# Optimization experiments

Measured on AMD Instinct MI355X. Metric: run time of the kernel, lower is better.

The kernel has to match this reference:

```python
import jax, jax.numpy as jnp
import numpy as np

OUTERCUTOFF = 5.0  # seqm_parameters['pair_outer_cutoff']
LENGTH_CONV = 1.8897261258369282  # Angstrom -> Bohr (constants.length_conversion_factor)
NMOL, MOLSIZE = 1024, 128


def setup_inputs() -> dict:
    key = jax.random.key(0)
    k1, k2 = jax.random.split(key)
    species = jax.random.randint(k1, (NMOL, MOLSIZE), 0, 9).astype(jnp.int32)
    coordinates = jax.random.uniform(k2, (NMOL, MOLSIZE, 3), dtype=jnp.float32) * 20.0
    # core charges indexed by atomic number (0=blank, H=1, ..., F=9)
    tore = jnp.array([0.0, 1.0, 0.0, 1.0, 2.0, 3.0, 4.0, 5.0, 6.0, 7.0], dtype=jnp.float32)
    return {"species": species, "coordinates": coordinates, "tore": tore}


def reference(species, coordinates, tore):
    nmol, molsize = species.shape
    nonblank = species > 0                               # (nmol, molsize)
    flat_nb = nonblank.reshape(-1)
    atom_index = jnp.arange(nmol * molsize, dtype=jnp.int32)
    real_atoms = atom_index[flat_nb]                     # compaction (eager, data-dependent)
    n_real = real_atoms.shape[0]
    inv_real_atoms = jnp.zeros((nmol * molsize,), jnp.int32).at[real_atoms].set(
        jnp.arange(n_real, dtype=jnp.int32))
    Z = species.reshape(-1)[real_atoms]
    nHeavy = jnp.sum(species > 1, axis=1)
    nHydro = jnp.sum(species == 1, axis=1)
    nocc = (jnp.sum(tore[species], axis=1) / 2.0).reshape(-1).astype(jnp.int32)
    t1 = (jnp.arange(molsize, dtype=jnp.int32) * (molsize + 1))[None, :]
    t2 = (jnp.arange(nmol, dtype=jnp.int32) * molsize ** 2)[:, None]
    maskd = (t1 + t2).reshape(-1)[real_atoms]
    atom_molid = jnp.repeat(jnp.arange(nmol, dtype=jnp.int32), molsize)[flat_nb]
    # pair bookkeeping: [i, a, b] with first=atom a, second=atom b
    nonblank_pairs = (nonblank[:, None, :] & nonblank[:, :, None]).reshape(-1)
    ai = atom_index.reshape(nmol, molsize)
    pair_first = jnp.broadcast_to(ai[:, :, None], (nmol, molsize, molsize)).reshape(-1)
    pair_second = jnp.broadcast_to(ai[:, None, :], (nmol, molsize, molsize)).reshape(-1)
    # paircoord_raw[i, a, b] = coord[i, b] - coord[i, a]
    paircoord_raw = (coordinates[:, None, :, :] - coordinates[:, :, None, :]).reshape(-1, 3)
    pairdist_raw = jnp.linalg.norm(paircoord_raw, axis=1)
    close_pairs = pairdist_raw < OUTERCUTOFF
    pairs = (pair_first < pair_second) & nonblank_pairs & close_pairs
    pidx = jnp.where(pairs)[0]
    paircoord = paircoord_raw[pidx]
    pairdist = pairdist_raw[pidx]
    rij = pairdist * LENGTH_CONV
    idxi = inv_real_atoms[pair_first[pidx]]
    idxj = inv_real_atoms[pair_second[pidx]]
    ni = Z[idxi]
    nj = Z[idxj]
    xij = paircoord / pairdist[:, None]
    mask = real_atoms[idxi] * molsize + real_atoms[idxj] % molsize
    pair_molid = atom_molid[idxi]
    return (nmol, molsize, nHeavy, nHydro, nocc, Z, maskd, atom_molid,
            mask, pair_molid, ni, nj, idxi, idxj, xij, rij)
```

## Files before the change

### kernel.cpp

```cpp
#include <hip/hip_runtime.h>
#include <hip/hip_bf16.h>

#define NMOL 1024
#define MOLSIZE 128


__device__ __forceinline__ float pair_dist(float ax, float ay, float az,
                                           float bx, float by, float bz,
                                           float& dx, float& dy, float& dz) {
    dx = __fsub_rn(bx, ax);
    dy = __fsub_rn(by, ay);
    dz = __fsub_rn(bz, az);
    float d2 = __fadd_rn(__fadd_rn(__fmul_rn(dx, dx), __fmul_rn(dy, dy)), __fmul_rn(dz, dz));
    return __fsqrt_rn(d2);
}

__global__ __launch_bounds__(256) void k_count(const int* __restrict__ species,
                                               const float* __restrict__ coord,
                                               const float* __restrict__ tore,
                                               float* __restrict__ out,
                                               int* __restrict__ cnt_real,
                                               int* __restrict__ pair_tot,
                                               unsigned long long* __restrict__ bal_g) {
    __shared__ float cx[MOLSIZE], cy[MOLSIZE], cz[MOLSIZE];
    __shared__ unsigned long long bal_s[256];
    __shared__ int sH[2], sY[2], sN[2];
    __shared__ float sT[2];
    __shared__ int wpair[4];
    int m = blockIdx.x, t = threadIdx.x;
    int lane = t & 63, w = t >> 6;
    if (t < MOLSIZE) {
        int f = m * MOLSIZE + t;
        int s = species[f];
        bool nb = (s > 0);
        float x = coord[3 * f + 0], y = coord[3 * f + 1], z = coord[3 * f + 2];
        float sent = 1.0e30f * (float)(t + 1);
        cx[t] = nb ? x : sent;
        cy[t] = nb ? y : sent;
        cz[t] = nb ? z : sent;
        int h = (s > 1) ? 1 : 0, yy = (s == 1) ? 1 : 0, nn = nb ? 1 : 0;
        float tv = tore[s];
        for (int d = 32; d > 0; d >>= 1) {
            h += __shfl_down(h, d);
            yy += __shfl_down(yy, d);
            nn += __shfl_down(nn, d);
            tv += __shfl_down(tv, d);
        }
        if (lane == 0) { sH[w] = h; sY[w] = yy; sN[w] = nn; sT[w] = tv; }
    }
    __syncthreads();
    if (t == 0) {
        out[2 + m] = (float)(sH[0] + sH[1]);
        out[2 + NMOL + m] = (float)(sY[0] + sY[1]);
        out[2 + 2 * NMOL + m] = (float)((int)((sT[0] + sT[1]) * 0.5f));
        cnt_real[m] = sN[0] + sN[1];
        if (m == 0) { out[0] = (float)NMOL; out[1] = (float)MOLSIZE; }
    }
    float bxl = cx[lane], byl = cy[lane], bzl = cz[lane];
    float bxh = cx[64 + lane], byh = cy[64 + lane], bzh = cz[64 + lane];
    int wcount = 0;
    for (int j = 0; j < 32; ++j) {
        int a = w + 4 * j;
        float ax = cx[a], ay = cy[a], az = cz[a];
        unsigned long long mb0 = 0ull, mb1 = 0ull;
        if (a < 63) {
            float dx, dy, dz;
            float dist = pair_dist(ax, ay, az, bxl, byl, bzl, dx, dy, dz);
            mb0 = __ballot((lane > a) && (dist < 5.0f));
        }
        if (a < 127) {
            float dx, dy, dz;
            float dist = pair_dist(ax, ay, az, bxh, byh, bzh, dx, dy, dz);
            mb1 = __ballot(((64 + lane) > a) && (dist < 5.0f));
        }
        if (lane == 0) { bal_s[2 * a] = mb0; bal_s[2 * a + 1] = mb1; }
        wcount += __popcll(mb0) + __popcll(mb1);
    }
    if (lane == 0) wpair[w] = wcount;
    __syncthreads();
    if (t == 0) pair_tot[m] = wpair[0] + wpair[1] + wpair[2] + wpair[3];
    bal_g[m * 256 + t] = bal_s[t];
}

__global__ __launch_bounds__(256) void k_scatter(const int* __restrict__ species,
                                                 const float* __restrict__ coord,
                                                 const int* __restrict__ cnt_real,
                                                 const int* __restrict__ pair_tot,
                                                 const unsigned long long* __restrict__ bal_g,
                                                 float* __restrict__ out) {
    __shared__ float cx[MOLSIZE], cy[MOLSIZE], cz[MOLSIZE], spf[MOLSIZE];
    __shared__ int iv[MOLSIZE];
    __shared__ unsigned long long bal_s[256];
    __shared__ int sIncl[256];
    __shared__ int wtot[4];
    __shared__ int redALT[4], redAALL[4], redPLT[4], redPALL[4];
    __shared__ int wc0s;
    int m = blockIdx.x, t = threadIdx.x;
    int lane = t & 63, w = t >> 6;

    unsigned long long bal = bal_g[m * 256 + t];
    bal_s[t] = bal;

    int4 ca = ((const int4*)cnt_real)[t];
    int4 cp = ((const int4*)pair_tot)[t];
    int i0 = 4 * t;
    int aLT = ((i0 + 0) < m ? ca.x : 0) + ((i0 + 1) < m ? ca.y : 0) +
              ((i0 + 2) < m ? ca.z : 0) + ((i0 + 3) < m ? ca.w : 0);
    int aALL = ca.x + ca.y + ca.z + ca.w;
    int pLT = ((i0 + 0) < m ? cp.x : 0) + ((i0 + 1) < m ? cp.y : 0) +
              ((i0 + 2) < m ? cp.z : 0) + ((i0 + 3) < m ? cp.w : 0);
    int pALL = cp.x + cp.y + cp.z + cp.w;
    for (int d = 32; d > 0; d >>= 1) {
        aLT += __shfl_down(aLT, d);
        aALL += __shfl_down(aALL, d);
        pLT += __shfl_down(pLT, d);
        pALL += __shfl_down(pALL, d);
    }
    if (lane == 0) { redALT[w] = aLT; redAALL[w] = aALL; redPLT[w] = pLT; redPALL[w] = pALL; }

    int s_at = 0;
    unsigned long long amb = 0ull;
    if (t < MOLSIZE) {
        int f = m * MOLSIZE + t;
        s_at = species[f];
        cx[t] = coord[3 * f + 0];
        cy[t] = coord[3 * f + 1];
        cz[t] = coord[3 * f + 2];
        spf[t] = (float)s_at;
        amb = __ballot(s_at > 0);
        if (t == 0) wc0s = __popcll(amb);
    }
    int v = __popcll(bal);
    int cval = v;
    for (int d = 1; d < 64; d <<= 1) {
        int u = __shfl_up(v, d);
        if (lane >= d) v += u;
    }
    (void)cval;
    if (lane == 63) wtot[w] = v;
    __syncthreads();

    int mol_base_m = redALT[0] + redALT[1] + redALT[2] + redALT[3];
    int n_real     = redAALL[0] + redAALL[1] + redAALL[2] + redAALL[3];
    int qbase      = redPLT[0] + redPLT[1] + redPLT[2] + redPLT[3];
    int npairs     = redPALL[0] + redPALL[1] + redPALL[2] + redPALL[3];

    if (t < MOLSIZE && s_at > 0) {
        int rank = __popcll(amb & ((1ull << lane) - 1ull)) + ((w == 1) ? wc0s : 0);
        int g = mol_base_m + rank;
        iv[t] = g;
        out[3074 + g] = (float)s_at;
        out[3074 + n_real + g] = (float)(t * (MOLSIZE + 1) + m * (MOLSIZE * MOLSIZE));
        out[3074 + 2 * n_real + g] = (float)m;
    }
    int add = 0;
    for (int ww = 0; ww < w; ++ww) add += wtot[ww];
    sIncl[t] = v + add;
    __syncthreads();
    int np_mol = sIncl[255];

    int offP = 3074 + 3 * n_real;
    float* pm0 = out + offP;
    float* pm1 = pm0 + npairs;
    float* pm2 = pm1 + npairs;
    float* pm3 = pm2 + npairs;
    float* pm4 = pm3 + npairs;
    float* pm5 = pm4 + npairs;
    float* px  = pm5 + npairs;
    float* pr  = px + 3 * npairs;
    float fm = (float)m;

    for (int q = t; q < np_mol; q += 256) {
        int c = 0;
        if (sIncl[c + 127] <= q) c += 128;
        if (sIncl[c + 63] <= q) c += 64;
        if (sIncl[c + 31] <= q) c += 32;
        if (sIncl[c + 15] <= q) c += 16;
        if (sIncl[c + 7] <= q) c += 8;
        if (sIncl[c + 3] <= q) c += 4;
        if (sIncl[c + 1] <= q) c += 2;
        if (sIncl[c] <= q) c += 1;
        int r = q - (c ? sIncl[c - 1] : 0);
        unsigned long long mb = bal_s[c];
        unsigned int cur = (unsigned int)mb;
        int idx = 0;
        int cc = __popc(cur);
        if (r >= cc) { r -= cc; idx = 32; cur = (unsigned int)(mb >> 32); }
        cc = __popc(cur & 0xFFFFu); if (r >= cc) { r -= cc; idx += 16; cur >>= 16; }
        cc = __popc(cur & 0xFFu);   if (r >= cc) { r -= cc; idx += 8;  cur >>= 8; }
        cc = __popc(cur & 0xFu);    if (r >= cc) { r -= cc; idx += 4;  cur >>= 4; }
        cc = __popc(cur & 0x3u);    if (r >= cc) { r -= cc; idx += 2;  cur >>= 2; }
        cc = cur & 1u;              if (r >= cc) { idx += 1; }
        int a = c >> 1;
        int b = ((c & 1) << 6) | idx;
        float dx, dy, dz;
        float dist = pair_dist(cx[a], cy[a], cz[a], cx[b], cy[b], cz[b], dx, dy, dz);
        int Q = qbase + q;
        pm0[Q] = (float)(m * (MOLSIZE * MOLSIZE) + a * MOLSIZE + b);
        pm1[Q] = fm;
        pm2[Q] = spf[a];
        pm3[Q] = spf[b];
        pm4[Q] = (float)iv[a];
        pm5[Q] = (float)iv[b];
        px[3 * Q + 0] = __fdiv_rn(dx, dist);
        px[3 * Q + 1] = __fdiv_rn(dy, dist);
        px[3 * Q + 2] = __fdiv_rn(dz, dist);
        pr[Q] = __fmul_rn(dist, 1.8897261258369282f);
    }
}

extern "C" void kernel_launch(void* const* d_in, const int* in_sizes, int n_in,
                              void* d_out, int out_size, void* d_ws, size_t ws_size,
                              hipStream_t stream) {
    const int* species = (const int*)d_in[0];
    const float* coords = (const float*)d_in[1];
    const float* tore = (const float*)d_in[2];
    float* out = (float*)d_out;
    int* ws = (int*)d_ws;

    int* cnt_real = ws;
    int* pair_tot = ws + 1024;
    unsigned long long* bal_g = (unsigned long long*)(ws + 2048);

    k_count<<<NMOL, 256, 0, stream>>>(species, coords, tore, out, cnt_real, pair_tot, bal_g);
    k_scatter<<<NMOL, 256, 0, stream>>>(species, coords, cnt_real, pair_tot, bal_g, out);
}
```

Measured before the change: 79.16 us.

## Fuse count and scatter kernels using cross-block published counts with spin-wait

Merges the counting and scatter kernels into one kernel. Each block publishes its real-atom and pair counts packed into a flagged word in global memory, then spins until every block's word is set before computing global offsets. This removes the second launch and the global round trip of ballot masks and coordinates. The cost is a memset, spinning, and a reliance on all 1024 blocks being co-resident, which launch_bounds(256,4) is meant to make likely on a 256-CU part; if they are not co-resident the kernel can deadlock. Pair counts are packed into 13 bits, which limits how many pairs a molecule may have.

```diff
diff --git a/kernel.cpp b/kernel.cpp
--- a/kernel.cpp
+++ b/kernel.cpp
@@ -1,5 +1,4 @@
 #include <hip/hip_runtime.h>
-#include <hip/hip_bf16.h>
 
 #define NMOL 1024
 #define MOLSIZE 128
@@ -15,31 +14,40 @@
     return __fsqrt_rn(d2);
 }
 
-__global__ __launch_bounds__(256) void k_count(const int* __restrict__ species,
-                                               const float* __restrict__ coord,
-                                               const float* __restrict__ tore,
-                                               float* __restrict__ out,
-                                               int* __restrict__ cnt_real,
-                                               int* __restrict__ pair_tot,
-                                               unsigned long long* __restrict__ bal_g) {
-    __shared__ float cx[MOLSIZE], cy[MOLSIZE], cz[MOLSIZE];
+__global__ __launch_bounds__(256, 4) void k_fused(const int* __restrict__ species,
+                                                  const float* __restrict__ coord,
+                                                  const float* __restrict__ tore,
+                                                  float* __restrict__ out,
+                                                  unsigned int* __restrict__ pub) {
+    __shared__ float cx[MOLSIZE], cy[MOLSIZE], cz[MOLSIZE], spf[MOLSIZE];
+    __shared__ int iv[MOLSIZE];
     __shared__ unsigned long long bal_s[256];
+    __shared__ int sIncl[256];
     __shared__ int sH[2], sY[2], sN[2];
     __shared__ float sT[2];
-    __shared__ int wpair[4];
+    __shared__ int wpair[4], wtot[4];
+    __shared__ int redALT[4], redAALL[4], redPLT[4], redPALL[4];
+    __shared__ int wc0s;
+
     int m = blockIdx.x, t = threadIdx.x;
     int lane = t & 63, w = t >> 6;
+
+    int s_at = 0;
+    unsigned long long amb = 0ull;
     if (t < MOLSIZE) {
         int f = m * MOLSIZE + t;
-        int s = species[f];
-        bool nb = (s > 0);
+        s_at = species[f];
+        bool nb = (s_at > 0);
         float x = coord[3 * f + 0], y = coord[3 * f + 1], z = coord[3 * f + 2];
         float sent = 1.0e30f * (float)(t + 1);
         cx[t] = nb ? x : sent;
         cy[t] = nb ? y : sent;
         cz[t] = nb ? z : sent;
-        int h = (s > 1) ? 1 : 0, yy = (s == 1) ? 1 : 0, nn = nb ? 1 : 0;
-        float tv = tore[s];
+        spf[t] = (float)s_at;
+        amb = __ballot(nb);
+        if (t == 0) wc0s = __popcll(amb);
+        int h = (s_at > 1) ? 1 : 0, yy = (s_at == 1) ? 1 : 0, nn = nb ? 1 : 0;
+        float tv = tore[s_at];
         for (int d = 32; d > 0; d >>= 1) {
             h += __shfl_down(h, d);
             yy += __shfl_down(yy, d);
@@ -53,9 +61,9 @@
         out[2 + m] = (float)(sH[0] + sH[1]);
         out[2 + NMOL + m] = (float)(sY[0] + sY[1]);
         out[2 + 2 * NMOL + m] = (float)((int)((sT[0] + sT[1]) * 0.5f));
-        cnt_real[m] = sN[0] + sN[1];
         if (m == 0) { out[0] = (float)NMOL; out[1] = (float)MOLSIZE; }
     }
+
     float bxl = cx[lane], byl = cy[lane], bzl = cz[lane];
     float bxh = cx[64 + lane], byh = cy[64 + lane], bzh = cz[64 + lane];
     int wcount = 0;
@@ -78,38 +86,50 @@
     }
     if (lane == 0) wpair[w] = wcount;
     __syncthreads();
-    if (t == 0) pair_tot[m] = wpair[0] + wpair[1] + wpair[2] + wpair[3];
-    bal_g[m * 256 + t] = bal_s[t];
-}
-
-__global__ __launch_bounds__(256) void k_scatter(const int* __restrict__ species,
-                                                 const float* __restrict__ coord,
-                                                 const int* __restrict__ cnt_real,
-                                                 const int* __restrict__ pair_tot,
-                                                 const unsigned long long* __restrict__ bal_g,
-                                                 float* __restrict__ out) {
-    __shared__ float cx[MOLSIZE], cy[MOLSIZE], cz[MOLSIZE], spf[MOLSIZE];
-    __shared__ int iv[MOLSIZE];
-    __shared__ unsigned long long bal_s[256];
-    __shared__ int sIncl[256];
-    __shared__ int wtot[4];
-    __shared__ int redALT[4], redAALL[4], redPLT[4], redPALL[4];
-    __shared__ int wc0s;
-    int m = blockIdx.x, t = threadIdx.x;
-    int lane = t & 63, w = t >> 6;
-
-    unsigned long long bal = bal_g[m * 256 + t];
-    bal_s[t] = bal;
-
-    int4 ca = ((const int4*)cnt_real)[t];
-    int4 cp = ((const int4*)pair_tot)[t];
+
+    if (t == 0) {
+        unsigned int nreal = (unsigned int)(sN[0] + sN[1]);
+        unsigned int ptot = (unsigned int)(wpair[0] + wpair[1] + wpair[2] + wpair[3]);
+        __hip_atomic_store(&pub[m], 0x80000000u | (ptot << 8) | nreal,
+                           __ATOMIC_RELAXED, __HIP_MEMORY_SCOPE_AGENT);
+    }
+
+    unsigned long long bal = bal_s[t];
+    int v = __popcll(bal);
+    for (int d = 1; d < 64; d <<= 1) {
+        int u = __shfl_up(v, d);
+        if (lane >= d) v += u;
+    }
+    if (lane == 63) wtot[w] = v;
+    if (t < MOLSIZE && s_at > 0)
+        iv[t] = __popcll(amb & ((1ull << lane) - 1ull)) + ((w == 1) ? wc0s : 0);
+    __syncthreads();
+    int add = 0;
+    for (int ww = 0; ww < w; ++ww) add += wtot[ww];
+    sIncl[t] = v + add;
+
+    unsigned int pw[4];
+#pragma unroll
+    for (int k = 0; k < 4; ++k) {
+        unsigned int val = __hip_atomic_load(&pub[4 * t + k], __ATOMIC_RELAXED,
+                                             __HIP_MEMORY_SCOPE_AGENT);
+        while (!(val & 0x80000000u)) {
+            __builtin_amdgcn_s_sleep(1);
+            val = __hip_atomic_load(&pub[4 * t + k], __ATOMIC_RELAXED,
+                                    __HIP_MEMORY_SCOPE_AGENT);
+        }
+        pw[k] = val;
+    }
+    int aLT = 0, aALL = 0, pLT = 0, pALL = 0;
     int i0 = 4 * t;
-    int aLT = ((i0 + 0) < m ? ca.x : 0) + ((i0 + 1) < m ? ca.y : 0) +
-              ((i0 + 2) < m ? ca.z : 0) + ((i0 + 3) < m ? ca.w : 0);
-    int aALL = ca.x + ca.y + ca.z + ca.w;
-    int pLT = ((i0 + 0) < m ? cp.x : 0) + ((i0 + 1) < m ? cp.y : 0) +
-              ((i0 + 2) < m ? cp.z : 0) + ((i0 + 3) < m ? cp.w : 0);
-    int pALL = cp.x + cp.y + cp.z + cp.w;
+#pragma unroll
+    for (int k = 0; k < 4; ++k) {
+        int real = (int)(pw[k] & 0xFFu);
+        int pr = (int)((pw[k] >> 8) & 0x1FFFu);
+        aALL += real;
+        pALL += pr;
+        if (i0 + k < m) { aLT += real; pLT += pr; }
+    }
     for (int d = 32; d > 0; d >>= 1) {
         aLT += __shfl_down(aLT, d);
         aALL += __shfl_down(aALL, d);
@@ -117,46 +137,19 @@
         pALL += __shfl_down(pALL, d);
     }
     if (lane == 0) { redALT[w] = aLT; redAALL[w] = aALL; redPLT[w] = pLT; redPALL[w] = pALL; }
-
-    int s_at = 0;
-    unsigned long long amb = 0ull;
-    if (t < MOLSIZE) {
-        int f = m * MOLSIZE + t;
-        s_at = species[f];
-        cx[t] = coord[3 * f + 0];
-        cy[t] = coord[3 * f + 1];
-        cz[t] = coord[3 * f + 2];
-        spf[t] = (float)s_at;
-        amb = __ballot(s_at > 0);
-        if (t == 0) wc0s = __popcll(amb);
-    }
-    int v = __popcll(bal);
-    int cval = v;
-    for (int d = 1; d < 64; d <<= 1) {
-        int u = __shfl_up(v, d);
-        if (lane >= d) v += u;
-    }
-    (void)cval;
-    if (lane == 63) wtot[w] = v;
-    __syncthreads();
-
-    int mol_base_m = redALT[0] + redALT[1] + redALT[2] + redALT[3];
-    int n_real     = redAALL[0] + redAALL[1] + redAALL[2] + redAALL[3];
-    int qbase      = redPLT[0] + redPLT[1] + redPLT[2] + redPLT[3];
-    int npairs     = redPALL[0] + redPALL[1] + redPALL[2] + redPALL[3];
+    __syncthreads();
+
+    int mol_base = redALT[0] + redALT[1] + redALT[2] + redALT[3];
+    int n_real   = redAALL[0] + redAALL[1] + redAALL[2] + redAALL[3];
+    int qbase    = redPLT[0] + redPLT[1] + redPLT[2] + redPLT[3];
+    int npairs   = redPALL[0] + redPALL[1] + redPALL[2] + redPALL[3];
 
     if (t < MOLSIZE && s_at > 0) {
-        int rank = __popcll(amb & ((1ull << lane) - 1ull)) + ((w == 1) ? wc0s : 0);
-        int g = mol_base_m + rank;
-        iv[t] = g;
-        out[3074 + g] = (float)s_at;
+        int g = mol_base + iv[t];
+        out[3074 + g] = spf[t];
         out[3074 + n_real + g] = (float)(t * (MOLSIZE + 1) + m * (MOLSIZE * MOLSIZE));
         out[3074 + 2 * n_real + g] = (float)m;
     }
-    int add = 0;
-    for (int ww = 0; ww < w; ++ww) add += wtot[ww];
-    sIncl[t] = v + add;
-    __syncthreads();
     int np_mol = sIncl[255];
 
     int offP = 3074 + 3 * n_real;
@@ -200,8 +193,8 @@
         pm1[Q] = fm;
         pm2[Q] = spf[a];
         pm3[Q] = spf[b];
-        pm4[Q] = (float)iv[a];
-        pm5[Q] = (float)iv[b];
+        pm4[Q] = (float)(mol_base + iv[a]);
+        pm5[Q] = (float)(mol_base + iv[b]);
         px[3 * Q + 0] = __fdiv_rn(dx, dist);
         px[3 * Q + 1] = __fdiv_rn(dy, dist);
         px[3 * Q + 2] = __fdiv_rn(dz, dist);
@@ -216,12 +209,8 @@
     const float* coords = (const float*)d_in[1];
     const float* tore = (const float*)d_in[2];
     float* out = (float*)d_out;
-    int* ws = (int*)d_ws;
-
-    int* cnt_real = ws;
-    int* pair_tot = ws + 1024;
-    unsigned long long* bal_g = (unsigned long long*)(ws + 2048);
-
-    k_count<<<NMOL, 256, 0, stream>>>(species, coords, tore, out, cnt_real, pair_tot, bal_g);
-    k_scatter<<<NMOL, 256, 0, stream>>>(species, coords, cnt_real, pair_tot, bal_g, out);
+    unsigned int* pub = (unsigned int*)d_ws;
+
+    hipMemsetAsync(pub, 0, NMOL * sizeof(unsigned int), stream);
+    k_fused<<<NMOL, 256, 0, stream>>>(species, coords, tore, out, pub);
 }
```

Result: slower. 84.31 us (+6.5%).
